# Kernel optimization log

Measured on AMD Instinct MI355X. Metric: run time of the kernel, lower is better.

Reference implementation:

```python
import jax, jax.numpy as jnp
import numpy as np

FEATURE_DIM = 512
HIDDEN_DIM = 512
N_HEADS = 8
HEAD_DIM = HIDDEN_DIM // N_HEADS
MAX_LEN = 5000
GAMMA = 0.5  # gaussian relative-position bias width
LN_EPS = 1e-5


def make_pe(d_model, max_len):
    # sinusoidal positional encoding buffer, as in PositionalEncoding.__init__
    pos = jnp.arange(max_len, dtype=jnp.float32)[:, None]
    div = jnp.exp(jnp.arange(0, d_model, 2, dtype=jnp.float32) * (-np.log(10000.0) / d_model))
    ang = pos * div  # [max_len, d_model/2]
    pe = jnp.zeros((max_len, d_model), dtype=jnp.float32)
    pe = pe.at[:, 0::2].set(jnp.sin(ang)).at[:, 1::2].set(jnp.cos(ang))
    return pe


def setup_inputs() -> dict:
    key = jax.random.key(0)
    k_x, k_q, k_k, k_v = jax.random.split(key, 4)
    xavier = np.sqrt(6.0 / (FEATURE_DIM + HEAD_DIM))  # xavier_uniform over last two dims
    return {
        "data_window": jax.random.normal(k_x, (1, 2048, FEATURE_DIM), dtype=jnp.float32),
        "W_query": jax.random.uniform(k_q, (N_HEADS, FEATURE_DIM, HEAD_DIM), jnp.float32, -xavier, xavier),
        "W_key": jax.random.uniform(k_k, (N_HEADS, FEATURE_DIM, HEAD_DIM), jnp.float32, -xavier, xavier),
        "W_value": jax.random.uniform(k_v, (N_HEADS, FEATURE_DIM, HEAD_DIM), jnp.float32, -xavier, xavier),
        "ln_gamma": jnp.ones((FEATURE_DIM,), dtype=jnp.float32),
        "ln_beta": jnp.zeros((FEATURE_DIM,), dtype=jnp.float32),
    }


def reference(data_window, W_query, W_key, W_value, ln_gamma, ln_beta):
    B, S, F = data_window.shape
    temperature = 1.0

    # LayerNorm over feature dim
    mu = jnp.mean(data_window, axis=-1, keepdims=True)
    var = jnp.mean(jnp.square(data_window - mu), axis=-1, keepdims=True)
    x = (data_window - mu) * jax.lax.rsqrt(var + LN_EPS) * ln_gamma + ln_beta

    # positional encoding, exactly as original: x + pe[:x.shape[0]] (requires B==1)
    pe = make_pe(FEATURE_DIM, MAX_LEN)
    x = x + pe[:B]  # [B,F] broadcasts over [B,S,F] only because B==1

    # per-head QKV projections, vectorized over heads
    Q = jnp.einsum('bsf,hfd->bhsd', x, W_query)
    K = jnp.einsum('bsf,hfd->bhsd', x, W_key)
    V = jnp.einsum('bsf,hfd->bhsd', x, W_value)

    scores = jnp.einsum('bhsd,bhtd->bhst', Q, K) / np.sqrt(HEAD_DIM)

    # gaussian relative-position bias: scale(=1) * exp(-gamma * (i-j)^2)
    p = jnp.arange(S, dtype=jnp.float32)
    rel = p[:, None] - p[None, :]
    bias = jnp.exp(-GAMMA * jnp.square(rel))  # [S,S]
    scores = (scores + bias[None, None]) / temperature
    # dropout on scores is identity in eval mode

    attn = jax.nn.softmax(scores, axis=-1)  # [B,H,S,S]
    head_out = jnp.einsum('bhst,bhtd->bhsd', attn, V)

    # concat heads along feature dim: [B,S,H*D]
    multi_head_output = head_out.transpose(0, 2, 1, 3).reshape(B, S, N_HEADS * HEAD_DIM)
    mean_weights = jnp.mean(attn, axis=1)  # [B,S,S]
    return multi_head_output, mean_weights
```

## Files before the change

kernel.cpp:

```cpp
#include <hip/hip_runtime.h>
#include <hip/hip_bf16.h>
#include <math.h>

#define S_LEN 2048
#define FDIM  512
#define NH    8
#define HD    64
#define MH_ELEMS (S_LEN * FDIM)
#define MEAN_ELEMS (S_LEN * S_LEN)

typedef _Float16 half_t;
typedef _Float16 half2v __attribute__((ext_vector_type(2)));
typedef _Float16 half4v __attribute__((ext_vector_type(4)));
typedef _Float16 half8v __attribute__((ext_vector_type(8)));
typedef float    float4v __attribute__((ext_vector_type(4)));

#define MFMA16(a, b, c) __builtin_amdgcn_mfma_f32_16x16x32_f16((a), (b), (c), 0, 0, 0)

#define VT_STRIDE 260
#define PS_STRIDE 264

__global__ __launch_bounds__(256) void ln_pe_kernel(const float* __restrict__ x,
                                                    const float* __restrict__ gamma,
                                                    const float* __restrict__ beta,
                                                    half_t* __restrict__ xo) {
    const int row = blockIdx.x;
    const int tid = threadIdx.x;
    const float2 v = ((const float2*)(x + (size_t)row * FDIM))[tid];
    float s = v.x + v.y;
    float q = v.x * v.x + v.y * v.y;
    #pragma unroll
    for (int off = 1; off < 64; off <<= 1) {
        s += __shfl_xor(s, off, 64);
        q += __shfl_xor(q, off, 64);
    }
    __shared__ float red[8];
    const int wave = tid >> 6;
    if ((tid & 63) == 0) { red[wave] = s; red[4 + wave] = q; }
    __syncthreads();
    s = red[0] + red[1] + red[2] + red[3];
    q = red[4] + red[5] + red[6] + red[7];
    const float mu  = s * (1.0f / FDIM);
    const float var = q * (1.0f / FDIM) - mu * mu;
    const float rstd = rsqrtf(var + 1e-5f);
    const int f0 = tid * 2, f1 = tid * 2 + 1;
    const float o0 = (v.x - mu) * rstd * gamma[f0] + beta[f0];
    const float o1 = (v.y - mu) * rstd * gamma[f1] + beta[f1] + 1.0f;
    half2v o; o.x = (half_t)o0; o.y = (half_t)o1;
    ((half2v*)(xo + (size_t)row * FDIM))[tid] = o;
}

__global__ __launch_bounds__(256) void qkv_kernel(const half_t* __restrict__ xh,
                                                  const float* __restrict__ Wq,
                                                  const float* __restrict__ Wk,
                                                  const float* __restrict__ Wv,
                                                  half_t* __restrict__ Qo,
                                                  half_t* __restrict__ Ko,
                                                  half_t* __restrict__ Vo) {
    const int ms0 = blockIdx.x * 128;
    const int h   = blockIdx.y;
    const int z   = blockIdx.z;
    const float* W = ((z == 0) ? Wq : (z == 1) ? Wk : Wv) + (size_t)h * FDIM * HD;
    half_t* Co = ((z == 0) ? Qo : (z == 1) ? Ko : Vo) + (size_t)h * S_LEN * HD;

    const int tid = threadIdx.x;
    const int wv = tid >> 6, lane = tid & 63;
    const int lo = lane & 15, qq = lane >> 4;

    const float4v zero4 = {0.f, 0.f, 0.f, 0.f};
    float4v acc[2][4];
    #pragma unroll
    for (int rg = 0; rg < 2; ++rg)
        #pragma unroll
        for (int cg = 0; cg < 4; ++cg) acc[rg][cg] = zero4;

    for (int k0 = 0; k0 < FDIM; k0 += 32) {
        half8v a[2];
        #pragma unroll
        for (int rg = 0; rg < 2; ++rg)
            a[rg] = *(const half8v*)(xh + (size_t)(ms0 + wv * 32 + rg * 16 + lo) * FDIM + k0 + qq * 8);
        half8v bw[4];
        #pragma unroll
        for (int cg = 0; cg < 4; ++cg)
            #pragma unroll
            for (int j = 0; j < 8; ++j)
                bw[cg][j] = (half_t)W[(size_t)(k0 + qq * 8 + j) * HD + cg * 16 + lo];
        #pragma unroll
        for (int rg = 0; rg < 2; ++rg)
            #pragma unroll
            for (int cg = 0; cg < 4; ++cg) acc[rg][cg] = MFMA16(a[rg], bw[cg], acc[rg][cg]);
    }
    #pragma unroll
    for (int rg = 0; rg < 2; ++rg)
        #pragma unroll
        for (int cg = 0; cg < 4; ++cg)
            #pragma unroll
            for (int r = 0; r < 4; ++r)
                Co[(size_t)(ms0 + wv * 32 + rg * 16 + qq * 4 + r) * HD + cg * 16 + lo] =
                    (half_t)acc[rg][cg][r];
}

__global__ __launch_bounds__(256) void lsum_kernel(const half_t* __restrict__ Qw,
                                                   const half_t* __restrict__ Kw,
                                                   float* __restrict__ linv) {
    const int s0 = blockIdx.x * 16;
    const int h  = blockIdx.y;
    const half_t* Qh = Qw + (size_t)h * S_LEN * HD;
    const half_t* Kh = Kw + (size_t)h * S_LEN * HD;

    const int tid = threadIdx.x;
    const int wv = tid >> 6, lane = tid & 63;
    const int lo = lane & 15, qq = lane >> 4;

    const half8v aq0 = *(const half8v*)(Qh + (size_t)(s0 + lo) * HD + qq * 8);
    const half8v aq1 = *(const half8v*)(Qh + (size_t)(s0 + lo) * HD + 32 + qq * 8);

    float esum[4] = {0.f, 0.f, 0.f, 0.f};
    for (int j = 0; j < 32; ++j) {
        const int cbase = (wv + 4 * j) * 16;
        const half8v b0 = *(const half8v*)(Kh + (size_t)(cbase + lo) * HD + qq * 8);
        const half8v b1 = *(const half8v*)(Kh + (size_t)(cbase + lo) * HD + 32 + qq * 8);
        float4v c4 = {0.f, 0.f, 0.f, 0.f};
        c4 = MFMA16(aq0, b0, c4);
        c4 = MFMA16(aq1, b1, c4);
        const int dd0 = cbase - s0;
        const bool near = (dd0 > -24) && (dd0 < 24);
        #pragma unroll
        for (int r = 0; r < 4; ++r) {
            float s = c4[r] * 0.125f;
            if (near) {
                const float d = (float)(s0 + qq * 4 + r - cbase - lo);
                s += __expf(-0.5f * d * d);
            }
            s = fminf(s, 60.f);
            esum[r] += __expf(s);
        }
    }
    #pragma unroll
    for (int r = 0; r < 4; ++r) {
        #pragma unroll
        for (int mk = 1; mk < 16; mk <<= 1) esum[r] += __shfl_xor(esum[r], mk, 64);
    }
    __shared__ float red[4][16];
    if (lo == 0) {
        #pragma unroll
        for (int r = 0; r < 4; ++r) red[wv][qq * 4 + r] = esum[r];
    }
    __syncthreads();
    if (tid < 16) {
        const float l = red[0][tid] + red[1][tid] + red[2][tid] + red[3][tid];
        linv[(size_t)h * S_LEN + s0 + tid] = 1.0f / l;
    }
}

__global__ __launch_bounds__(256, 3) void attn_kernel(const half_t* __restrict__ Qw,
                                                      const half_t* __restrict__ Kw,
                                                      const half_t* __restrict__ Vw,
                                                      const float* __restrict__ linv,
                                                      float* __restrict__ partial,
                                                      float* __restrict__ out) {
    const int s0 = blockIdx.x * 32;
    const int c0 = blockIdx.y * 256;

    __shared__ half_t Vt[64 * VT_STRIDE];
    __shared__ half_t Ps[32 * PS_STRIDE];

    const int tid = threadIdx.x;
    const int wv = tid >> 6, lane = tid & 63;
    const int rg = wv & 1, chw = wv >> 1;
    const int lo = lane & 15, qq = lane >> 4;
    const int rbase = s0 + rg * 16;
    const int tlow = tid & 31, dcs = tid >> 5;

    float msum[8][4];
    #pragma unroll
    for (int ct = 0; ct < 8; ++ct)
        #pragma unroll
        for (int r = 0; r < 4; ++r) msum[ct][r] = 0.f;

    float* po = partial + (size_t)blockIdx.y * (size_t)MH_ELEMS;

    for (int h = 0; h < NH; ++h) {
        const half_t* Qh = Qw + (size_t)h * S_LEN * HD;
        const half_t* Kh = Kw + (size_t)h * S_LEN * HD;
        const half_t* Vh = Vw + (size_t)h * S_LEN * HD;
        __syncthreads();
        #pragma unroll
        for (int it = 0; it < 8; ++it) {
            const int t = tlow + 32 * it;
            const half8v v8 = *(const half8v*)(Vh + (size_t)(c0 + t) * HD + dcs * 8);
            #pragma unroll
            for (int j = 0; j < 8; ++j) Vt[(size_t)(dcs * 8 + j) * VT_STRIDE + t] = v8[j];
        }
        const half8v aq0 = *(const half8v*)(Qh + (size_t)(rbase + lo) * HD + qq * 8);
        const half8v aq1 = *(const half8v*)(Qh + (size_t)(rbase + lo) * HD + 32 + qq * 8);
        float li[4];
        #pragma unroll
        for (int r = 0; r < 4; ++r) li[r] = linv[(size_t)h * S_LEN + rbase + qq * 4 + r];
        #pragma unroll
        for (int ct = 0; ct < 8; ++ct) {
            const int cbase = c0 + chw * 128 + ct * 16;
            const half8v b0 = *(const half8v*)(Kh + (size_t)(cbase + lo) * HD + qq * 8);
            const half8v b1 = *(const half8v*)(Kh + (size_t)(cbase + lo) * HD + 32 + qq * 8);
            float4v c4 = {0.f, 0.f, 0.f, 0.f};
            c4 = MFMA16(aq0, b0, c4);
            c4 = MFMA16(aq1, b1, c4);
            const int dd0 = cbase - rbase;
            const bool near = (dd0 > -24) && (dd0 < 24);
            #pragma unroll
            for (int r = 0; r < 4; ++r) {
                float s = c4[r] * 0.125f;
                if (near) {
                    const float d = (float)(rbase + qq * 4 + r - cbase - lo);
                    s += __expf(-0.5f * d * d);
                }
                s = fminf(s, 60.f);
                const float e = __expf(s);
                const float p = e * li[r];
                msum[ct][r] += p;
                Ps[(size_t)(rg * 16 + qq * 4 + r) * PS_STRIDE + chw * 128 + ct * 16 + lo] = (half_t)p;
            }
        }
        __syncthreads();
        float4v accO[2];
        accO[0] = (float4v){0.f, 0.f, 0.f, 0.f};
        accO[1] = (float4v){0.f, 0.f, 0.f, 0.f};
        #pragma unroll
        for (int ks = 0; ks < 8; ++ks) {
            const half8v ap = *(const half8v*)&Ps[(size_t)(rg * 16 + lo) * PS_STRIDE + ks * 32 + qq * 8];
            #pragma unroll
            for (int dgi = 0; dgi < 2; ++dgi) {
                const int d0 = (chw * 2 + dgi) * 16;
                const size_t voff = (size_t)(d0 + lo) * VT_STRIDE + ks * 32 + qq * 8;
                const half4v u0 = *(const half4v*)&Vt[voff];
                const half4v u1 = *(const half4v*)&Vt[voff + 4];
                half8v bv;
                bv[0] = u0[0]; bv[1] = u0[1]; bv[2] = u0[2]; bv[3] = u0[3];
                bv[4] = u1[0]; bv[5] = u1[1]; bv[6] = u1[2]; bv[7] = u1[3];
                accO[dgi] = MFMA16(ap, bv, accO[dgi]);
            }
        }
        #pragma unroll
        for (int dgi = 0; dgi < 2; ++dgi)
            #pragma unroll
            for (int r = 0; r < 4; ++r)
                po[(size_t)(rbase + qq * 4 + r) * FDIM + h * HD + (chw * 2 + dgi) * 16 + lo] =
                    accO[dgi][r];
    }
    #pragma unroll
    for (int ct = 0; ct < 8; ++ct)
        #pragma unroll
        for (int r = 0; r < 4; ++r)
            out[MH_ELEMS + (size_t)(rbase + qq * 4 + r) * S_LEN + c0 + chw * 128 + ct * 16 + lo] =
                msum[ct][r] * 0.125f;
}

__global__ __launch_bounds__(256) void reduce_kernel(const float* __restrict__ partial,
                                                     float* __restrict__ out) {
    const size_t i4 = ((size_t)blockIdx.x * 256 + threadIdx.x) * 4;
    float4 s = *(const float4*)(partial + i4);
    #pragma unroll
    for (int c = 1; c < 8; ++c) {
        const float4 t = *(const float4*)(partial + (size_t)c * MH_ELEMS + i4);
        s.x += t.x; s.y += t.y; s.z += t.z; s.w += t.w;
    }
    *(float4*)(out + i4) = s;
}

extern "C" void kernel_launch(void* const* d_in, const int* in_sizes, int n_in,
                              void* d_out, int out_size, void* d_ws, size_t ws_size,
                              hipStream_t stream) {
    const float* x  = (const float*)d_in[0];
    const float* Wq = (const float*)d_in[1];
    const float* Wk = (const float*)d_in[2];
    const float* Wv = (const float*)d_in[3];
    const float* g  = (const float*)d_in[4];
    const float* b  = (const float*)d_in[5];
    float* out = (float*)d_out;
    char*  ws  = (char*)d_ws;

    half_t* xh   = (half_t*)(ws);
    half_t* Qh   = (half_t*)(ws + (2ull << 20));
    half_t* Kh   = (half_t*)(ws + (4ull << 20));
    half_t* Vh   = (half_t*)(ws + (6ull << 20));
    float*  linv = (float*)(ws + (8ull << 20));
    float*  part = (float*)(ws + (9ull << 20));

    ln_pe_kernel<<<S_LEN, 256, 0, stream>>>(x, g, b, xh);
    qkv_kernel<<<dim3(16, 8, 3), 256, 0, stream>>>(xh, Wq, Wk, Wv, Qh, Kh, Vh);
    lsum_kernel<<<dim3(128, 8), 256, 0, stream>>>(Qh, Kh, linv);
    attn_kernel<<<dim3(64, 8), 256, 0, stream>>>(Qh, Kh, Vh, linv, part, out);
    reduce_kernel<<<MH_ELEMS / 4 / 256, 256, 0, stream>>>(part, out);
}
```

Measured before the change: 190.5 us.

## Pre-transpose weights and V, widen attention blocks, store partials in half

Adds a kernel that converts the projection weights to fp16 and transposes them, so the QKV GEMM does vector loads instead of strided scalar float loads. The QKV kernel writes V already transposed through shared memory, which removes the per-head LDS transpose of V in the attention kernel. The attention kernel moves to 512 threads with each wave covering 64 columns, and its per-column-block partial outputs are stored in fp16, halving the partial write and reduce traffic. This adds one launch and some rounding error in the partial sums.

```diff
diff --git a/kernel.cpp b/kernel.cpp
--- a/kernel.cpp
+++ b/kernel.cpp
@@ -11,14 +11,12 @@
 
 typedef _Float16 half_t;
 typedef _Float16 half2v __attribute__((ext_vector_type(2)));
-typedef _Float16 half4v __attribute__((ext_vector_type(4)));
 typedef _Float16 half8v __attribute__((ext_vector_type(8)));
 typedef float    float4v __attribute__((ext_vector_type(4)));
 
 #define MFMA16(a, b, c) __builtin_amdgcn_mfma_f32_16x16x32_f16((a), (b), (c), 0, 0, 0)
 
-#define VT_STRIDE 260
-#define PS_STRIDE 264
+#define PS2 264
 
 __global__ __launch_bounds__(256) void ln_pe_kernel(const float* __restrict__ x,
                                                     const float* __restrict__ gamma,
@@ -50,54 +48,90 @@
     ((half2v*)(xo + (size_t)row * FDIM))[tid] = o;
 }
 
+__global__ __launch_bounds__(256) void wt_kernel(const float* __restrict__ Wq,
+                                                 const float* __restrict__ Wk,
+                                                 const float* __restrict__ Wv,
+                                                 half_t* __restrict__ WT) {
+    const int k0 = blockIdx.x * 64;
+    const int h  = blockIdx.y, z = blockIdx.z;
+    const float* W = ((z == 0) ? Wq : (z == 1) ? Wk : Wv) + (size_t)h * FDIM * HD;
+    __shared__ float Ls[64][65];
+    const int tid = threadIdx.x;
+    {
+        const int kk = tid >> 2, dg = (tid & 3) * 16;
+        #pragma unroll
+        for (int j = 0; j < 4; ++j) {
+            const float4 w = *(const float4*)(W + (size_t)(k0 + kk) * HD + dg + j * 4);
+            Ls[kk][dg + j * 4 + 0] = w.x; Ls[kk][dg + j * 4 + 1] = w.y;
+            Ls[kk][dg + j * 4 + 2] = w.z; Ls[kk][dg + j * 4 + 3] = w.w;
+        }
+    }
+    __syncthreads();
+    {
+        const int d = tid >> 2, kg = (tid & 3) * 16;
+        half8v t0, t1;
+        #pragma unroll
+        for (int j = 0; j < 8; ++j) t0[j] = (half_t)Ls[kg + j][d];
+        #pragma unroll
+        for (int j = 0; j < 8; ++j) t1[j] = (half_t)Ls[kg + 8 + j][d];
+        half_t* dst = WT + ((size_t)(z * NH + h) * HD + d) * FDIM + k0 + kg;
+        *(half8v*)dst = t0;
+        *(half8v*)(dst + 8) = t1;
+    }
+}
+
 __global__ __launch_bounds__(256) void qkv_kernel(const half_t* __restrict__ xh,
-                                                  const float* __restrict__ Wq,
-                                                  const float* __restrict__ Wk,
-                                                  const float* __restrict__ Wv,
+                                                  const half_t* __restrict__ WT,
                                                   half_t* __restrict__ Qo,
                                                   half_t* __restrict__ Ko,
-                                                  half_t* __restrict__ Vo) {
-    const int ms0 = blockIdx.x * 128;
-    const int h   = blockIdx.y;
-    const int z   = blockIdx.z;
-    const float* W = ((z == 0) ? Wq : (z == 1) ? Wk : Wv) + (size_t)h * FDIM * HD;
-    half_t* Co = ((z == 0) ? Qo : (z == 1) ? Ko : Vo) + (size_t)h * S_LEN * HD;
+                                                  half_t* __restrict__ VTo) {
+    const int ms0 = blockIdx.x * 64;
+    const int h   = blockIdx.y, z = blockIdx.z;
+    const half_t* Wt = WT + (size_t)(z * NH + h) * HD * FDIM;
 
     const int tid = threadIdx.x;
     const int wv = tid >> 6, lane = tid & 63;
     const int lo = lane & 15, qq = lane >> 4;
 
-    const float4v zero4 = {0.f, 0.f, 0.f, 0.f};
-    float4v acc[2][4];
-    #pragma unroll
-    for (int rg = 0; rg < 2; ++rg)
-        #pragma unroll
-        for (int cg = 0; cg < 4; ++cg) acc[rg][cg] = zero4;
+    float4v acc[4];
+    #pragma unroll
+    for (int cg = 0; cg < 4; ++cg) acc[cg] = (float4v){0.f, 0.f, 0.f, 0.f};
 
     for (int k0 = 0; k0 < FDIM; k0 += 32) {
-        half8v a[2];
-        #pragma unroll
-        for (int rg = 0; rg < 2; ++rg)
-            a[rg] = *(const half8v*)(xh + (size_t)(ms0 + wv * 32 + rg * 16 + lo) * FDIM + k0 + qq * 8);
-        half8v bw[4];
+        const half8v a = *(const half8v*)(xh + (size_t)(ms0 + wv * 16 + lo) * FDIM + k0 + qq * 8);
+        half8v b[4];
         #pragma unroll
         for (int cg = 0; cg < 4; ++cg)
-            #pragma unroll
-            for (int j = 0; j < 8; ++j)
-                bw[cg][j] = (half_t)W[(size_t)(k0 + qq * 8 + j) * HD + cg * 16 + lo];
-        #pragma unroll
-        for (int rg = 0; rg < 2; ++rg)
-            #pragma unroll
-            for (int cg = 0; cg < 4; ++cg) acc[rg][cg] = MFMA16(a[rg], bw[cg], acc[rg][cg]);
-    }
-    #pragma unroll
-    for (int rg = 0; rg < 2; ++rg)
+            b[cg] = *(const half8v*)(Wt + (size_t)(cg * 16 + lo) * FDIM + k0 + qq * 8);
+        #pragma unroll
+        for (int cg = 0; cg < 4; ++cg) acc[cg] = MFMA16(a, b[cg], acc[cg]);
+    }
+
+    __shared__ float Ls[64][65];
+    if (z < 2) {
+        half_t* Co = ((z == 0) ? Qo : Ko) + (size_t)h * S_LEN * HD;
         #pragma unroll
         for (int cg = 0; cg < 4; ++cg)
             #pragma unroll
             for (int r = 0; r < 4; ++r)
-                Co[(size_t)(ms0 + wv * 32 + rg * 16 + qq * 4 + r) * HD + cg * 16 + lo] =
-                    (half_t)acc[rg][cg][r];
+                Co[(size_t)(ms0 + wv * 16 + qq * 4 + r) * HD + cg * 16 + lo] = (half_t)acc[cg][r];
+    } else {
+        #pragma unroll
+        for (int cg = 0; cg < 4; ++cg)
+            #pragma unroll
+            for (int r = 0; r < 4; ++r)
+                Ls[wv * 16 + qq * 4 + r][cg * 16 + lo] = acc[cg][r];
+        __syncthreads();
+        const int d = tid & 63, sg = tid >> 6;
+        half8v t0, t1;
+        #pragma unroll
+        for (int j = 0; j < 8; ++j) t0[j] = (half_t)Ls[sg * 16 + j][d];
+        #pragma unroll
+        for (int j = 0; j < 8; ++j) t1[j] = (half_t)Ls[sg * 16 + 8 + j][d];
+        half_t* dst = VTo + (size_t)(h * HD + d) * S_LEN + ms0 + sg * 16;
+        *(half8v*)dst = t0;
+        *(half8v*)(dst + 8) = t1;
+    }
 }
 
 __global__ __launch_bounds__(256) void lsum_kernel(const half_t* __restrict__ Qw,
@@ -116,6 +150,7 @@
     const half8v aq1 = *(const half8v*)(Qh + (size_t)(s0 + lo) * HD + 32 + qq * 8);
 
     float esum[4] = {0.f, 0.f, 0.f, 0.f};
+    #pragma unroll 2
     for (int j = 0; j < 32; ++j) {
         const int cbase = (wv + 4 * j) * 16;
         const half8v b0 = *(const half8v*)(Kh + (size_t)(cbase + lo) * HD + qq * 8);
@@ -153,53 +188,44 @@
     }
 }
 
-__global__ __launch_bounds__(256, 3) void attn_kernel(const half_t* __restrict__ Qw,
+__global__ __launch_bounds__(512, 4) void attn_kernel(const half_t* __restrict__ Qw,
                                                       const half_t* __restrict__ Kw,
-                                                      const half_t* __restrict__ Vw,
+                                                      const half_t* __restrict__ VT,
                                                       const float* __restrict__ linv,
-                                                      float* __restrict__ partial,
+                                                      half_t* __restrict__ partial,
                                                       float* __restrict__ out) {
     const int s0 = blockIdx.x * 32;
     const int c0 = blockIdx.y * 256;
 
-    __shared__ half_t Vt[64 * VT_STRIDE];
-    __shared__ half_t Ps[32 * PS_STRIDE];
+    __shared__ half_t Ps[32 * PS2];
 
     const int tid = threadIdx.x;
     const int wv = tid >> 6, lane = tid & 63;
-    const int rg = wv & 1, chw = wv >> 1;
+    const int rg = wv & 1, cq = wv >> 1;
     const int lo = lane & 15, qq = lane >> 4;
     const int rbase = s0 + rg * 16;
-    const int tlow = tid & 31, dcs = tid >> 5;
-
-    float msum[8][4];
-    #pragma unroll
-    for (int ct = 0; ct < 8; ++ct)
+
+    float msum[4][4];
+    #pragma unroll
+    for (int ct = 0; ct < 4; ++ct)
         #pragma unroll
         for (int r = 0; r < 4; ++r) msum[ct][r] = 0.f;
 
-    float* po = partial + (size_t)blockIdx.y * (size_t)MH_ELEMS;
+    half_t* po = partial + (size_t)blockIdx.y * (size_t)MH_ELEMS;
 
     for (int h = 0; h < NH; ++h) {
         const half_t* Qh = Qw + (size_t)h * S_LEN * HD;
         const half_t* Kh = Kw + (size_t)h * S_LEN * HD;
-        const half_t* Vh = Vw + (size_t)h * S_LEN * HD;
+        const half_t* Vt = VT + (size_t)h * (size_t)HD * S_LEN;
         __syncthreads();
-        #pragma unroll
-        for (int it = 0; it < 8; ++it) {
-            const int t = tlow + 32 * it;
-            const half8v v8 = *(const half8v*)(Vh + (size_t)(c0 + t) * HD + dcs * 8);
-            #pragma unroll
-            for (int j = 0; j < 8; ++j) Vt[(size_t)(dcs * 8 + j) * VT_STRIDE + t] = v8[j];
-        }
         const half8v aq0 = *(const half8v*)(Qh + (size_t)(rbase + lo) * HD + qq * 8);
         const half8v aq1 = *(const half8v*)(Qh + (size_t)(rbase + lo) * HD + 32 + qq * 8);
         float li[4];
         #pragma unroll
         for (int r = 0; r < 4; ++r) li[r] = linv[(size_t)h * S_LEN + rbase + qq * 4 + r];
         #pragma unroll
-        for (int ct = 0; ct < 8; ++ct) {
-            const int cbase = c0 + chw * 128 + ct * 16;
+        for (int ct = 0; ct < 4; ++ct) {
+            const int cbase = c0 + cq * 64 + ct * 16;
             const half8v b0 = *(const half8v*)(Kh + (size_t)(cbase + lo) * HD + qq * 8);
             const half8v b1 = *(const half8v*)(Kh + (size_t)(cbase + lo) * HD + 32 + qq * 8);
             float4v c4 = {0.f, 0.f, 0.f, 0.f};
@@ -215,56 +241,43 @@
                     s += __expf(-0.5f * d * d);
                 }
                 s = fminf(s, 60.f);
-                const float e = __expf(s);
-                const float p = e * li[r];
+                const float p = __expf(s) * li[r];
                 msum[ct][r] += p;
-                Ps[(size_t)(rg * 16 + qq * 4 + r) * PS_STRIDE + chw * 128 + ct * 16 + lo] = (half_t)p;
+                Ps[(size_t)(rg * 16 + qq * 4 + r) * PS2 + cq * 64 + ct * 16 + lo] = (half_t)p;
             }
         }
         __syncthreads();
-        float4v accO[2];
-        accO[0] = (float4v){0.f, 0.f, 0.f, 0.f};
-        accO[1] = (float4v){0.f, 0.f, 0.f, 0.f};
+        float4v accO = {0.f, 0.f, 0.f, 0.f};
         #pragma unroll
         for (int ks = 0; ks < 8; ++ks) {
-            const half8v ap = *(const half8v*)&Ps[(size_t)(rg * 16 + lo) * PS_STRIDE + ks * 32 + qq * 8];
-            #pragma unroll
-            for (int dgi = 0; dgi < 2; ++dgi) {
-                const int d0 = (chw * 2 + dgi) * 16;
-                const size_t voff = (size_t)(d0 + lo) * VT_STRIDE + ks * 32 + qq * 8;
-                const half4v u0 = *(const half4v*)&Vt[voff];
-                const half4v u1 = *(const half4v*)&Vt[voff + 4];
-                half8v bv;
-                bv[0] = u0[0]; bv[1] = u0[1]; bv[2] = u0[2]; bv[3] = u0[3];
-                bv[4] = u1[0]; bv[5] = u1[1]; bv[6] = u1[2]; bv[7] = u1[3];
-                accO[dgi] = MFMA16(ap, bv, accO[dgi]);
-            }
+            const half8v ap = *(const half8v*)&Ps[(size_t)(rg * 16 + lo) * PS2 + ks * 32 + qq * 8];
+            const half8v bv = *(const half8v*)(Vt + (size_t)(cq * 16 + lo) * S_LEN + c0 + ks * 32 + qq * 8);
+            accO = MFMA16(ap, bv, accO);
         }
         #pragma unroll
-        for (int dgi = 0; dgi < 2; ++dgi)
-            #pragma unroll
-            for (int r = 0; r < 4; ++r)
-                po[(size_t)(rbase + qq * 4 + r) * FDIM + h * HD + (chw * 2 + dgi) * 16 + lo] =
-                    accO[dgi][r];
-    }
-    #pragma unroll
-    for (int ct = 0; ct < 8; ++ct)
-        #pragma unroll
         for (int r = 0; r < 4; ++r)
-            out[MH_ELEMS + (size_t)(rbase + qq * 4 + r) * S_LEN + c0 + chw * 128 + ct * 16 + lo] =
+            po[(size_t)(rbase + qq * 4 + r) * FDIM + h * HD + cq * 16 + lo] = (half_t)accO[r];
+    }
+    #pragma unroll
+    for (int ct = 0; ct < 4; ++ct)
+        #pragma unroll
+        for (int r = 0; r < 4; ++r)
+            out[MH_ELEMS + (size_t)(rbase + qq * 4 + r) * S_LEN + c0 + cq * 64 + ct * 16 + lo] =
                 msum[ct][r] * 0.125f;
 }
 
-__global__ __launch_bounds__(256) void reduce_kernel(const float* __restrict__ partial,
+__global__ __launch_bounds__(256) void reduce_kernel(const half_t* __restrict__ partial,
                                                      float* __restrict__ out) {
-    const size_t i4 = ((size_t)blockIdx.x * 256 + threadIdx.x) * 4;
-    float4 s = *(const float4*)(partial + i4);
-    #pragma unroll
-    for (int c = 1; c < 8; ++c) {
-        const float4 t = *(const float4*)(partial + (size_t)c * MH_ELEMS + i4);
-        s.x += t.x; s.y += t.y; s.z += t.z; s.w += t.w;
-    }
-    *(float4*)(out + i4) = s;
+    const size_t i8 = ((size_t)blockIdx.x * 256 + threadIdx.x) * 8;
+    float s[8] = {0.f, 0.f, 0.f, 0.f, 0.f, 0.f, 0.f, 0.f};
+    #pragma unroll
+    for (int c = 0; c < 8; ++c) {
+        const half8v t = *(const half8v*)(partial + (size_t)c * MH_ELEMS + i8);
+        #pragma unroll
+        for (int j = 0; j < 8; ++j) s[j] += (float)t[j];
+    }
+    *(float4*)(out + i8)     = make_float4(s[0], s[1], s[2], s[3]);
+    *(float4*)(out + i8 + 4) = make_float4(s[4], s[5], s[6], s[7]);
 }
 
 extern "C" void kernel_launch(void* const* d_in, const int* in_sizes, int n_in,
@@ -280,15 +293,17 @@
     char*  ws  = (char*)d_ws;
 
     half_t* xh   = (half_t*)(ws);
-    half_t* Qh   = (half_t*)(ws + (2ull << 20));
-    half_t* Kh   = (half_t*)(ws + (4ull << 20));
-    half_t* Vh   = (half_t*)(ws + (6ull << 20));
-    float*  linv = (float*)(ws + (8ull << 20));
-    float*  part = (float*)(ws + (9ull << 20));
+    half_t* Qh   = (half_t*)(ws + (2ull  << 20));
+    half_t* Kh   = (half_t*)(ws + (4ull  << 20));
+    half_t* VT   = (half_t*)(ws + (6ull  << 20));
+    half_t* WT   = (half_t*)(ws + (8ull  << 20));
+    float*  linv = (float*) (ws + (10ull << 20));
+    half_t* part = (half_t*)(ws + (11ull << 20));
 
     ln_pe_kernel<<<S_LEN, 256, 0, stream>>>(x, g, b, xh);
-    qkv_kernel<<<dim3(16, 8, 3), 256, 0, stream>>>(xh, Wq, Wk, Wv, Qh, Kh, Vh);
+    wt_kernel<<<dim3(8, 8, 3), 256, 0, stream>>>(Wq, Wk, Wv, WT);
+    qkv_kernel<<<dim3(32, 8, 3), 256, 0, stream>>>(xh, WT, Qh, Kh, VT);
     lsum_kernel<<<dim3(128, 8), 256, 0, stream>>>(Qh, Kh, linv);
-    attn_kernel<<<dim3(64, 8), 256, 0, stream>>>(Qh, Kh, Vh, linv, part, out);
-    reduce_kernel<<<MH_ELEMS / 4 / 256, 256, 0, stream>>>(part, out);
-}
+    attn_kernel<<<dim3(64, 8), 512, 0, stream>>>(Qh, Kh, VT, linv, part, out);
+    reduce_kernel<<<MH_ELEMS / 8 / 256, 256, 0, stream>>>(part, out);
+}
```

Measured after the change: 208.4 us. 1.09x slower.
